# Performance work log

Measured on AMD Instinct MI355X. Metric: run time of the kernel, lower is better.

Reference implementation:

```python
import jax, jax.numpy as jnp
import numpy as np

NUM_CLASSES = 2
THRESHOLD = 0.5
NEGPOS_RATIO = 3
VAR0, VAR1 = 0.1, 0.2  # self.variance = [0.1, 0.2]


def point_form(priors):
    # [cx,cy,w,h] -> [xmin,ymin,xmax,ymax]
    return jnp.concatenate([priors[:, :2] - priors[:, 2:] / 2,
                            priors[:, :2] + priors[:, 2:] / 2], axis=1)


def jaccard(a, b):
    # a: [O,4], b: [P,4] point-form -> IoU [O,P]
    tl = jnp.maximum(a[:, None, :2], b[None, :, :2])
    br = jnp.minimum(a[:, None, 2:], b[None, :, 2:])
    wh = jnp.clip(br - tl, 0.0)
    inter = wh[..., 0] * wh[..., 1]
    area_a = ((a[:, 2] - a[:, 0]) * (a[:, 3] - a[:, 1]))[:, None]
    area_b = ((b[:, 2] - b[:, 0]) * (b[:, 3] - b[:, 1]))[None, :]
    return inter / (area_a + area_b - inter)


def encode(matched, priors):
    # matched: [P,4] point-form GT, priors: [P,4] center-size
    g_cxcy = ((matched[:, :2] + matched[:, 2:]) / 2 - priors[:, :2]) / (VAR0 * priors[:, 2:])
    g_wh = jnp.log((matched[:, 2:] - matched[:, :2]) / priors[:, 2:]) / VAR1
    return jnp.concatenate([g_cxcy, g_wh], axis=1)


def match_one(truths, labels, priors):
    # truths: [O,4], labels: [O], priors: [P,4]
    O = truths.shape[0]
    overlaps = jaccard(truths, point_form(priors))          # [O,P]
    best_prior_idx = jnp.argmax(overlaps, axis=1)           # [O] best prior per GT
    best_truth_overlap = jnp.max(overlaps, axis=0)          # [P]
    best_truth_idx = jnp.argmax(overlaps, axis=0)           # [P]
    # ensure each GT keeps its best prior
    best_truth_overlap = best_truth_overlap.at[best_prior_idx].set(2.0)
    best_truth_idx = best_truth_idx.at[best_prior_idx].set(jnp.arange(O))
    matches = truths[best_truth_idx]                        # [P,4]
    conf = labels[best_truth_idx].astype(jnp.int32)         # head label == 1
    conf = jnp.where(best_truth_overlap < THRESHOLD, 0, conf)
    loc = encode(matches, priors)                           # [P,4]
    return loc, conf


def setup_inputs() -> dict:
    key = jax.random.key(0)
    k1, k2, k3, k4, k5, k6 = jax.random.split(key, 6)
    B, P, O = 32, 32768, 32
    loc_data = jax.random.normal(k1, (B, P, 3), jnp.float32) * 0.1
    conf_data = jax.random.normal(k2, (B, P, 2), jnp.float32)
    cxy = jax.random.uniform(k3, (P, 2), jnp.float32, 0.1, 0.9)
    wh = jax.random.uniform(k4, (P, 2), jnp.float32, 0.05, 0.2)
    priors = jnp.concatenate([cxy, wh], axis=1)
    xy1 = jax.random.uniform(k5, (B, O, 2), jnp.float32, 0.0, 0.7)
    twh = jax.random.uniform(k6, (B, O, 2), jnp.float32, 0.05, 0.25)
    targets = jnp.concatenate([xy1, xy1 + twh, jnp.ones((B, O, 1), jnp.float32)], axis=2)
    return {"loc_data": loc_data, "conf_data": conf_data, "priors": priors, "targets": targets}


def reference(loc_data, conf_data, priors, targets):
    B, P, _ = loc_data.shape
    # convert_coord: [cx, cy, gw] -> [cx, cy, gw, gw]
    quard = jnp.stack([loc_data[..., 0], loc_data[..., 1],
                       loc_data[..., 2], loc_data[..., 2]], axis=-1)  # [B,P,4]
    truths = targets[..., :4]
    labels = targets[..., 4]
    loc_t, conf_t = jax.vmap(lambda t, l: match_one(t, l, priors))(truths, labels)
    pos = conf_t > 0                                         # [B,P]
    # localization smooth-L1 over positives (sum reduction)
    d = quard - loc_t
    ad = jnp.abs(d)
    sl1 = jnp.where(ad < 1.0, 0.5 * d * d, ad - 0.5)
    loss_l = jnp.sum(sl1 * pos[..., None].astype(sl1.dtype))
    # per-prior CE for hard-negative mining
    lse = jax.nn.logsumexp(conf_data, axis=-1)               # [B,P]
    picked = jnp.take_along_axis(conf_data, conf_t[..., None], axis=-1)[..., 0]
    ce = lse - picked                                        # [B,P]
    ce_mine = jnp.where(pos, 0.0, ce)
    # double argsort -> rank of each prior by mining loss (descending)
    loss_idx = jnp.argsort(-ce_mine, axis=1)
    idx_rank = jnp.argsort(loss_idx, axis=1)
    num_pos = jnp.sum(pos.astype(jnp.int32), axis=1, keepdims=True)  # [B,1]
    num_neg = jnp.minimum(NEGPOS_RATIO * num_pos, P - 1)
    neg = idx_rank < num_neg
    sel = jnp.logical_or(pos, neg)
    loss_c = jnp.sum(jnp.where(sel, ce, 0.0))
    N = jnp.sum(num_pos).astype(loss_l.dtype)
    return loss_l / N, loss_c / N
```

## Files before the change

### kernel.cpp

```cpp
#include <hip/hip_runtime.h>
#include <math.h>

#define Bn 32
#define Pn 32768
#define On 32
#define TPB 256
#define PPT 4
#define BP  (TPB * PPT)


__global__ __launch_bounds__(256) void matchA(const float4* __restrict__ priors,
                                              const float* __restrict__ targets,
                                              unsigned long long* __restrict__ bpm) {
    int bo = blockIdx.x, chunk = blockIdx.y;
    const float* t = targets + (size_t)bo * 5;
    float tx1 = t[0], ty1 = t[1], tx2 = t[2], ty2 = t[3];
    float area_a = (tx2 - tx1) * (ty2 - ty1);

    int base = chunk * (Pn / 4) + threadIdx.x;
    float bI[4] = {0.f, 0.f, 0.f, 0.f};
    float bU[4] = {1.f, 1.f, 1.f, 1.f};
    int   bp[4];
#pragma unroll
    for (int c = 0; c < 4; c++) bp[c] = base + 256 * c;

#pragma unroll 2
    for (int i = 0; i < 8; i++) {
#pragma unroll
        for (int c = 0; c < 4; c++) {
            int p = base + (i * 4 + c) * 256;
            float4 pr = priors[p];
            float px1 = pr.x - pr.z * 0.5f, py1 = pr.y - pr.w * 0.5f;
            float px2 = pr.x + pr.z * 0.5f, py2 = pr.y + pr.w * 0.5f;
            float ix1 = fmaxf(tx1, px1), iy1 = fmaxf(ty1, py1);
            float ix2 = fminf(tx2, px2), iy2 = fminf(ty2, py2);
            float iw = fmaxf(ix2 - ix1, 0.f), ih = fmaxf(iy2 - iy1, 0.f);
            float I = iw * ih;
            float U = area_a + (px2 - px1) * (py2 - py1) - I;
            if (I * bU[c] > bI[c] * U) { bI[c] = I; bU[c] = U; bp[c] = p; }
        }
    }
    unsigned long long key = 0ull;
#pragma unroll
    for (int c = 0; c < 4; c++) {
        float iou = bI[c] / bU[c];
        unsigned long long kc = ((unsigned long long)__float_as_uint(iou) << 32)
                              | (unsigned)(Pn - 1 - bp[c]);
        if (kc > key) key = kc;
    }

    __shared__ unsigned long long sk[256];
    sk[threadIdx.x] = key;
    __syncthreads();
    for (int s = 128; s > 0; s >>= 1) {
        if ((int)threadIdx.x < s) {
            unsigned long long o = sk[threadIdx.x + s];
            if (o > sk[threadIdx.x]) sk[threadIdx.x] = o;
        }
        __syncthreads();
    }
    if (threadIdx.x == 0) atomicMax(&bpm[bo], sk[0]);
}

__global__ __launch_bounds__(256) void matchB(const float* __restrict__ loc,
                                              const float2* __restrict__ conf2,
                                              const float4* __restrict__ priors,
                                              const float* __restrict__ targets,
                                              const unsigned long long* __restrict__ bpm,
                                              float* __restrict__ ce_mine,
                                              int* __restrict__ num_pos,
                                              float* __restrict__ loss_l_t,
                                              float* __restrict__ ce_t,
                                              int* __restrict__ np_tot) {
    int b = blockIdx.y;
    int base = blockIdx.x * BP;
    int tid = threadIdx.x;

    __shared__ float4 tb[On];
    __shared__ float  ta[On], lb[On];
    __shared__ int    forced[BP];
    __shared__ float  sred[12];

#pragma unroll
    for (int j = 0; j < PPT; j++) forced[tid + 256 * j] = -1;
    int sp = -1;
    if (tid < On) {
        const float* t = targets + ((size_t)b * On + tid) * 5;
        float x1 = t[0], y1 = t[1], x2 = t[2], y2 = t[3];
        tb[tid] = make_float4(x1, y1, x2, y2);
        ta[tid] = (x2 - x1) * (y2 - y1);
        lb[tid] = t[4];
        sp = Pn - 1 - (int)(bpm[b * On + tid] & 0xFFFFFFFFull);
    }
    __syncthreads();
    if (tid < On && sp >= base && sp < base + BP)
        atomicMax(&forced[sp - base], tid);
    __syncthreads();

    float px1[PPT], py1[PPT], px2[PPT], py2[PPT], ab[PPT], pcx[PPT], pcy[PPT], pw[PPT], ph[PPT];
#pragma unroll
    for (int j = 0; j < PPT; j++) {
        float4 pr = priors[base + tid + 256 * j];
        pcx[j] = pr.x; pcy[j] = pr.y; pw[j] = pr.z; ph[j] = pr.w;
        px1[j] = pr.x - pr.z * 0.5f; py1[j] = pr.y - pr.w * 0.5f;
        px2[j] = pr.x + pr.z * 0.5f; py2[j] = pr.y + pr.w * 0.5f;
        ab[j]  = (px2[j] - px1[j]) * (py2[j] - py1[j]);
    }

    float bI[PPT] = {0.f, 0.f, 0.f, 0.f};
    float bU[PPT] = {1.f, 1.f, 1.f, 1.f};
    int   bx[PPT] = {0, 0, 0, 0};
#pragma unroll 4
    for (int o = 0; o < On; o++) {
        float4 tt = tb[o];
        float  a  = ta[o];
#pragma unroll
        for (int j = 0; j < PPT; j++) {
            float ix1 = fmaxf(tt.x, px1[j]), iy1 = fmaxf(tt.y, py1[j]);
            float ix2 = fminf(tt.z, px2[j]), iy2 = fminf(tt.w, py2[j]);
            float iw = fmaxf(ix2 - ix1, 0.f), ih = fmaxf(iy2 - iy1, 0.f);
            float I = iw * ih;
            float U = a + ab[j] - I;
            if (I * bU[j] > bI[j] * U) { bI[j] = I; bU[j] = U; bx[j] = o; }
        }
    }

    float ll_s = 0.f, pce_s = 0.f, cnt_s = 0.f;
#pragma unroll
    for (int j = 0; j < PPT; j++) {
        int p = base + tid + 256 * j;
        int fo = forced[tid + 256 * j];
        int bidx = (fo >= 0) ? fo : bx[j];
        int cf;
        if (fo >= 0)                      cf = (int)lb[bidx];
        else if (bI[j] >= 0.5f * bU[j])   cf = (int)lb[bidx];
        else                              cf = 0;
        bool pos = cf > 0;

        if (pos) {
            float4 tt = tb[bidx];
            float g0 = ((tt.x + tt.z) * 0.5f - pcx[j]) / (0.1f * pw[j]);
            float g1 = ((tt.y + tt.w) * 0.5f - pcy[j]) / (0.1f * ph[j]);
            float g2 = __logf((tt.z - tt.x) / pw[j]) * 5.0f;
            float g3 = __logf((tt.w - tt.y) / ph[j]) * 5.0f;
            const float* lp = loc + ((size_t)b * Pn + p) * 3;
            float q0 = lp[0], q1 = lp[1], q2 = lp[2];
            float dd[4] = { q0 - g0, q1 - g1, q2 - g2, q2 - g3 };
#pragma unroll
            for (int i = 0; i < 4; i++) {
                float ad = fabsf(dd[i]);
                ll_s += (ad < 1.f) ? 0.5f * dd[i] * dd[i] : (ad - 0.5f);
            }
            cnt_s += 1.f;
        }

        float2 cc = conf2[(size_t)b * Pn + p];
        float m = fmaxf(cc.x, cc.y);
        float lse = m + __logf(__expf(cc.x - m) + __expf(cc.y - m));
        float ce = lse - (cf ? cc.y : cc.x);
        if (pos) { pce_s += ce; ce = 0.f; }
        ce_mine[(size_t)b * Pn + p] = fmaxf(ce, 0.f);
    }

#pragma unroll
    for (int off = 32; off > 0; off >>= 1) {
        ll_s  += __shfl_down(ll_s,  off, 64);
        pce_s += __shfl_down(pce_s, off, 64);
        cnt_s += __shfl_down(cnt_s, off, 64);
    }
    int lane = tid & 63, wv = tid >> 6;
    if (lane == 0) { sred[wv * 3] = ll_s; sred[wv * 3 + 1] = pce_s; sred[wv * 3 + 2] = cnt_s; }
    __syncthreads();
    if (tid == 0) {
        float llr = 0, pcer = 0, cntr = 0;
        for (int w = 0; w < 4; w++) { llr += sred[w*3]; pcer += sred[w*3+1]; cntr += sred[w*3+2]; }
        if (llr != 0.f)  atomicAdd(loss_l_t, llr);
        if (pcer != 0.f) atomicAdd(ce_t, pcer);
        int c = (int)cntr;
        if (c) { atomicAdd(&num_pos[b], c); atomicAdd(np_tot, c); }
    }
}

__global__ __launch_bounds__(1024) void topk(const float* __restrict__ ce_mine,
                                             const int* __restrict__ num_pos,
                                             float* __restrict__ ce_t) {
    int b = blockIdx.x, tid = threadIdx.x;
    const float4* v4 = (const float4*)(ce_mine + (size_t)b * Pn);
    float4 r[8];
#pragma unroll
    for (int i = 0; i < 8; i++) r[i] = v4[i * 1024 + tid];

    int k = 3 * num_pos[b];
    if (k > Pn - 1) k = Pn - 1;
    if (k <= 0) return;

    __shared__ int   scnt[16];
    __shared__ float ssum[16];
    __shared__ int   s_tot;

    unsigned lo = 0u, hi = 0x7F800000u;
    while (hi - lo > 1u) {
        unsigned mid = lo + ((hi - lo) >> 1);
        float mf = __uint_as_float(mid);
        int c = 0;
#pragma unroll
        for (int i = 0; i < 8; i++) {
            c += (r[i].x > mf) + (r[i].y > mf) + (r[i].z > mf) + (r[i].w > mf);
        }
#pragma unroll
        for (int off = 32; off > 0; off >>= 1) c += __shfl_down(c, off, 64);
        if ((tid & 63) == 0) scnt[tid >> 6] = c;
        __syncthreads();
        if (tid == 0) { int t = 0; for (int w = 0; w < 16; w++) t += scnt[w]; s_tot = t; }
        __syncthreads();
        if (s_tot >= k) lo = mid; else hi = mid;
    }
    float tv = __uint_as_float(hi);
    float s = 0.f; int c = 0;
#pragma unroll
    for (int i = 0; i < 8; i++) {
        if (r[i].x > tv) { s += r[i].x; c++; }
        if (r[i].y > tv) { s += r[i].y; c++; }
        if (r[i].z > tv) { s += r[i].z; c++; }
        if (r[i].w > tv) { s += r[i].w; c++; }
    }
#pragma unroll
    for (int off = 32; off > 0; off >>= 1) {
        s += __shfl_down(s, off, 64);
        c += __shfl_down(c, off, 64);
    }
    if ((tid & 63) == 0) { ssum[tid >> 6] = s; scnt[tid >> 6] = c; }
    __syncthreads();
    if (tid == 0) {
        float st = 0.f; int ct = 0;
        for (int w = 0; w < 16; w++) { st += ssum[w]; ct += scnt[w]; }
        atomicAdd(ce_t, st + (float)(k - ct) * tv);
    }
}

__global__ void finalize(const float* __restrict__ loss_l_t,
                         const float* __restrict__ ce_t,
                         const int* __restrict__ np_tot,
                         float* __restrict__ out) {
    float N = (float)(*np_tot);
    out[0] = *loss_l_t / N;
    out[1] = *ce_t / N;
}

extern "C" void kernel_launch(void* const* d_in, const int* in_sizes, int n_in,
                              void* d_out, int out_size, void* d_ws, size_t ws_size,
                              hipStream_t stream) {
    const float* loc     = (const float*)d_in[0];
    const float* conf    = (const float*)d_in[1];
    const float* priors  = (const float*)d_in[2];
    const float* targets = (const float*)d_in[3];
    float* out = (float*)d_out;

    char* ws = (char*)d_ws;
    unsigned long long* bpm = (unsigned long long*)ws;
    int*   num_pos  = (int*)(ws + 8192);
    float* loss_l_t = (float*)(ws + 8320);
    float* ce_t     = (float*)(ws + 8324);
    int*   np_tot   = (int*)(ws + 8328);
    float* ce_mine  = (float*)(ws + 16384);

    hipMemsetAsync(ws, 0, 16384, stream);

    hipLaunchKernelGGL(matchA, dim3(Bn * On, 4), dim3(256), 0, stream,
                       (const float4*)priors, targets, bpm);
    hipLaunchKernelGGL(matchB, dim3(Pn / BP, Bn), dim3(256), 0, stream,
                       loc, (const float2*)conf, (const float4*)priors, targets, bpm,
                       ce_mine, num_pos, loss_l_t, ce_t, np_tot);
    hipLaunchKernelGGL(topk, dim3(Bn), dim3(1024), 0, stream, ce_mine, num_pos, ce_t);
    hipLaunchKernelGGL(finalize, dim3(1), dim3(1), 0, stream, loss_l_t, ce_t, np_tot, out);
}
```

Baseline: 171.3 us.

## Tile matchA over GT groups, halve matchB work per thread, radix-select top-k

matchA now gives each block 8 ground-truth boxes and a 1024-prior chunk, so priors are loaded once and reused across those 8 boxes, and the reduction becomes wave shuffles plus shared and global atomicMax. matchB drops to 2 priors per thread, which doubles its grid to raise occupancy. The topk kernel swaps a ~31-iteration bisection, each step with two block barriers, for a 3-pass radix histogram select over the float bit patterns. This adds shared-memory atomic contention and a large shared histogram in exchange for fewer barriers.

```diff
diff --git a/kernel.cpp b/kernel.cpp
--- a/kernel.cpp
+++ b/kernel.cpp
@@ -5,61 +5,77 @@
 #define Pn 32768
 #define On 32
 #define TPB 256
-#define PPT 4
+#define PPT 2
 #define BP  (TPB * PPT)
-
+#define AG 8
+#define AC 1024
+
+
+__device__ __forceinline__ unsigned long long shfl_down_u64(unsigned long long v, int off) {
+    unsigned lo = (unsigned)(v & 0xFFFFFFFFull);
+    unsigned hi = (unsigned)(v >> 32);
+    lo = __shfl_down(lo, off, 64);
+    hi = __shfl_down(hi, off, 64);
+    return ((unsigned long long)hi << 32) | lo;
+}
 
 __global__ __launch_bounds__(256) void matchA(const float4* __restrict__ priors,
                                               const float* __restrict__ targets,
                                               unsigned long long* __restrict__ bpm) {
-    int bo = blockIdx.x, chunk = blockIdx.y;
-    const float* t = targets + (size_t)bo * 5;
-    float tx1 = t[0], ty1 = t[1], tx2 = t[2], ty2 = t[3];
-    float area_a = (tx2 - tx1) * (ty2 - ty1);
-
-    int base = chunk * (Pn / 4) + threadIdx.x;
-    float bI[4] = {0.f, 0.f, 0.f, 0.f};
-    float bU[4] = {1.f, 1.f, 1.f, 1.f};
-    int   bp[4];
-#pragma unroll
-    for (int c = 0; c < 4; c++) bp[c] = base + 256 * c;
-
-#pragma unroll 2
-    for (int i = 0; i < 8; i++) {
-#pragma unroll
-        for (int c = 0; c < 4; c++) {
-            int p = base + (i * 4 + c) * 256;
-            float4 pr = priors[p];
-            float px1 = pr.x - pr.z * 0.5f, py1 = pr.y - pr.w * 0.5f;
-            float px2 = pr.x + pr.z * 0.5f, py2 = pr.y + pr.w * 0.5f;
-            float ix1 = fmaxf(tx1, px1), iy1 = fmaxf(ty1, py1);
-            float ix2 = fminf(tx2, px2), iy2 = fminf(ty2, py2);
+    int g    = blockIdx.x;
+    int base = blockIdx.y * AC;
+    int tid  = threadIdx.x;
+
+    __shared__ float4 tb[AG];
+    __shared__ float  ta[AG];
+    __shared__ unsigned long long sbest[AG];
+
+    if (tid < AG) {
+        const float* t = targets + (size_t)(g * AG + tid) * 5;
+        float x1 = t[0], y1 = t[1], x2 = t[2], y2 = t[3];
+        tb[tid] = make_float4(x1, y1, x2, y2);
+        ta[tid] = (x2 - x1) * (y2 - y1);
+        sbest[tid] = 0ull;
+    }
+    __syncthreads();
+
+    float px1[4], py1[4], px2[4], py2[4], ab[4];
+#pragma unroll
+    for (int j = 0; j < 4; j++) {
+        float4 pr = priors[base + tid + 256 * j];
+        px1[j] = pr.x - pr.z * 0.5f; py1[j] = pr.y - pr.w * 0.5f;
+        px2[j] = pr.x + pr.z * 0.5f; py2[j] = pr.y + pr.w * 0.5f;
+        ab[j]  = (px2[j] - px1[j]) * (py2[j] - py1[j]);
+    }
+
+#pragma unroll
+    for (int o = 0; o < AG; o++) {
+        float4 tt = tb[o];
+        float  a  = ta[o];
+        float bI = 0.f, bU = 1.f;
+        int   bj = 0;
+#pragma unroll
+        for (int j = 0; j < 4; j++) {
+            float ix1 = fmaxf(tt.x, px1[j]), iy1 = fmaxf(tt.y, py1[j]);
+            float ix2 = fminf(tt.z, px2[j]), iy2 = fminf(tt.w, py2[j]);
             float iw = fmaxf(ix2 - ix1, 0.f), ih = fmaxf(iy2 - iy1, 0.f);
             float I = iw * ih;
-            float U = area_a + (px2 - px1) * (py2 - py1) - I;
-            if (I * bU[c] > bI[c] * U) { bI[c] = I; bU[c] = U; bp[c] = p; }
-        }
-    }
-    unsigned long long key = 0ull;
-#pragma unroll
-    for (int c = 0; c < 4; c++) {
-        float iou = bI[c] / bU[c];
-        unsigned long long kc = ((unsigned long long)__float_as_uint(iou) << 32)
-                              | (unsigned)(Pn - 1 - bp[c]);
-        if (kc > key) key = kc;
-    }
-
-    __shared__ unsigned long long sk[256];
-    sk[threadIdx.x] = key;
-    __syncthreads();
-    for (int s = 128; s > 0; s >>= 1) {
-        if ((int)threadIdx.x < s) {
-            unsigned long long o = sk[threadIdx.x + s];
-            if (o > sk[threadIdx.x]) sk[threadIdx.x] = o;
-        }
-        __syncthreads();
-    }
-    if (threadIdx.x == 0) atomicMax(&bpm[bo], sk[0]);
+            float U = a + ab[j] - I;
+            if (I * bU > bI * U) { bI = I; bU = U; bj = j; }
+        }
+        int p = base + tid + 256 * bj;
+        float iou = bI / bU;
+        unsigned long long key = ((unsigned long long)__float_as_uint(iou) << 32)
+                               | (unsigned)(Pn - 1 - p);
+#pragma unroll
+        for (int off = 32; off > 0; off >>= 1) {
+            unsigned long long other = shfl_down_u64(key, off);
+            if (other > key) key = other;
+        }
+        if ((tid & 63) == 0) atomicMax(&sbest[o], key);
+    }
+    __syncthreads();
+    if (tid < AG) atomicMax(&bpm[g * AG + tid], sbest[tid]);
 }
 
 __global__ __launch_bounds__(256) void matchB(const float* __restrict__ loc,
@@ -107,9 +123,9 @@
         ab[j]  = (px2[j] - px1[j]) * (py2[j] - py1[j]);
     }
 
-    float bI[PPT] = {0.f, 0.f, 0.f, 0.f};
-    float bU[PPT] = {1.f, 1.f, 1.f, 1.f};
-    int   bx[PPT] = {0, 0, 0, 0};
+    float bI[PPT] = {0.f, 0.f};
+    float bU[PPT] = {1.f, 1.f};
+    int   bx[PPT] = {0, 0};
 #pragma unroll 4
     for (int o = 0; o < On; o++) {
         float4 tt = tb[o];
@@ -194,47 +210,101 @@
     if (k > Pn - 1) k = Pn - 1;
     if (k <= 0) return;
 
+    __shared__ int hist[4][2048];
+    __shared__ int wavetot[16];
+    __shared__ int waveabove[16];
+    __shared__ unsigned long long wcand[16];
+    __shared__ unsigned s_lo;
+    __shared__ int s_ab;
+    __shared__ float ssum[16];
     __shared__ int   scnt[16];
-    __shared__ float ssum[16];
-    __shared__ int   s_tot;
-
-    unsigned lo = 0u, hi = 0x7F800000u;
-    while (hi - lo > 1u) {
-        unsigned mid = lo + ((hi - lo) >> 1);
-        float mf = __uint_as_float(mid);
-        int c = 0;
+
+    int lane = tid & 63, wv = tid >> 6;
+    unsigned LO = 0u;
+    int AB = 0;
+
+    const int shifts[3] = {20, 9, 0};
+    const int nbs[3]    = {2048, 2048, 512};
+
+#pragma unroll
+    for (int rd = 0; rd < 3; rd++) {
+        int shift = shifts[rd], nb = nbs[rd];
+        int* hf = &hist[0][0];
+        for (int i = tid; i < 4 * 2048; i += 1024) hf[i] = 0;
+        __syncthreads();
+        int* myh = hist[wv >> 2];
 #pragma unroll
         for (int i = 0; i < 8; i++) {
-            c += (r[i].x > mf) + (r[i].y > mf) + (r[i].z > mf) + (r[i].w > mf);
-        }
-#pragma unroll
-        for (int off = 32; off > 0; off >>= 1) c += __shfl_down(c, off, 64);
-        if ((tid & 63) == 0) scnt[tid >> 6] = c;
-        __syncthreads();
-        if (tid == 0) { int t = 0; for (int w = 0; w < 16; w++) t += scnt[w]; s_tot = t; }
-        __syncthreads();
-        if (s_tot >= k) lo = mid; else hi = mid;
-    }
-    float tv = __uint_as_float(hi);
+            float4 rv = r[i];
+            float vals[4] = {rv.x, rv.y, rv.z, rv.w};
+#pragma unroll
+            for (int q = 0; q < 4; q++) {
+                unsigned u = __float_as_uint(vals[q]);
+                unsigned bin = (u - LO) >> shift;
+                if (bin < (unsigned)nb) atomicAdd(&myh[bin], 1);
+            }
+        }
+        __syncthreads();
+        int c0 = hist[0][2*tid] + hist[1][2*tid] + hist[2][2*tid] + hist[3][2*tid];
+        int c1 = hist[0][2*tid+1] + hist[1][2*tid+1] + hist[2][2*tid+1] + hist[3][2*tid+1];
+        int local = c0 + c1;
+        int suf = local;
+#pragma unroll
+        for (int off = 1; off < 64; off <<= 1) {
+            int src = lane + off;
+            int o = __shfl(suf, src & 63, 64);
+            suf += (src < 64) ? o : 0;
+        }
+        if (lane == 0) wavetot[wv] = suf;
+        __syncthreads();
+        if (tid == 0) {
+            int acc = AB;
+            for (int w = 15; w >= 0; w--) { waveabove[w] = acc; acc += wavetot[w]; }
+        }
+        __syncthreads();
+        int S0 = waveabove[wv] + suf;
+        int S1 = S0 - c0;
+        int cand = -1; unsigned nab = 0;
+        if (S0 >= k) { cand = 2*tid;     nab = (unsigned)(S0 - c0); }
+        if (S1 >= k) { cand = 2*tid + 1; nab = (unsigned)(S1 - c1); }
+        unsigned long long pk = ((unsigned long long)(unsigned)(cand + 1) << 32) | nab;
+#pragma unroll
+        for (int off = 32; off > 0; off >>= 1) {
+            unsigned long long o = shfl_down_u64(pk, off);
+            if (o > pk) pk = o;
+        }
+        if (lane == 0) wcand[wv] = pk;
+        __syncthreads();
+        if (tid == 0) {
+            unsigned long long best = 0;
+            for (int w = 0; w < 16; w++) if (wcand[w] > best) best = wcand[w];
+            int ci = (int)(best >> 32) - 1;
+            s_lo = LO + ((unsigned)ci << shift);
+            s_ab = (int)(best & 0xFFFFFFFFu);
+        }
+        __syncthreads();
+        LO = s_lo; AB = s_ab;
+    }
+    float tau = __uint_as_float(LO);
     float s = 0.f; int c = 0;
 #pragma unroll
     for (int i = 0; i < 8; i++) {
-        if (r[i].x > tv) { s += r[i].x; c++; }
-        if (r[i].y > tv) { s += r[i].y; c++; }
-        if (r[i].z > tv) { s += r[i].z; c++; }
-        if (r[i].w > tv) { s += r[i].w; c++; }
+        if (r[i].x > tau) { s += r[i].x; c++; }
+        if (r[i].y > tau) { s += r[i].y; c++; }
+        if (r[i].z > tau) { s += r[i].z; c++; }
+        if (r[i].w > tau) { s += r[i].w; c++; }
     }
 #pragma unroll
     for (int off = 32; off > 0; off >>= 1) {
         s += __shfl_down(s, off, 64);
         c += __shfl_down(c, off, 64);
     }
-    if ((tid & 63) == 0) { ssum[tid >> 6] = s; scnt[tid >> 6] = c; }
+    if (lane == 0) { ssum[wv] = s; scnt[wv] = c; }
     __syncthreads();
     if (tid == 0) {
         float st = 0.f; int ct = 0;
         for (int w = 0; w < 16; w++) { st += ssum[w]; ct += scnt[w]; }
-        atomicAdd(ce_t, st + (float)(k - ct) * tv);
+        atomicAdd(ce_t, st + (float)(k - ct) * tau);
     }
 }
 
@@ -266,7 +336,7 @@
 
     hipMemsetAsync(ws, 0, 16384, stream);
 
-    hipLaunchKernelGGL(matchA, dim3(Bn * On, 4), dim3(256), 0, stream,
+    hipLaunchKernelGGL(matchA, dim3((Bn * On) / AG, Pn / AC), dim3(256), 0, stream,
                        (const float4*)priors, targets, bpm);
     hipLaunchKernelGGL(matchB, dim3(Pn / BP, Bn), dim3(256), 0, stream,
                        loc, (const float2*)conf, (const float4*)priors, targets, bpm,
```

Result: slower. 195.2 us (+13.9%).
